# Optimization experiments

Hardware: AMD Instinct MI355X
Metric: run time of the kernel (lower is better)

## Reference

```python
import jax, jax.numpy as jnp
import numpy as np

MAX_SEQ = 512
HIDDEN = 1024
E = 2048  # hidden * expansion_factor
S = 128
EPS = 1e-05


def _rope(x):
    # x: [b, n, 2, s]; rotate along sequence dim (dim=1 in the torch code)
    b, n, h, s = x.shape
    half = s // 2
    pos = jnp.arange(n, dtype=x.dtype)
    # torch: freq_seq = -arange(half)/half; inv_freq = 10000**(-freq_seq) = 10000**(arange/half)
    inv_freq = jnp.power(jnp.asarray(10000.0, x.dtype), jnp.arange(half, dtype=x.dtype) / half)
    sinusoid = pos[:, None] * inv_freq[None, :]          # [n, half]
    sin = jnp.sin(sinusoid)[None, :, None, :]            # [1, n, 1, half]
    cos = jnp.cos(sinusoid)[None, :, None, :]
    x1, x2 = jnp.split(x, 2, axis=-1)
    return jnp.concatenate([x1 * cos - x2 * sin, x2 * cos + x1 * sin], axis=-1)


def _rel_pos_bias(w, seq_len):
    # toeplitz construction (max_seq_length <= 512 branch)
    t = jnp.pad(w, (0, seq_len))                          # [3*seq_len - 1]
    t = jnp.tile(t, seq_len)[:-seq_len]                   # [seq_len*(3*seq_len-2)]
    t = t.reshape(seq_len, 3 * seq_len - 2)
    r = (2 * seq_len - 1) // 2
    return t[:, r:-r][None]                               # [1, seq_len, seq_len]


def setup_inputs() -> dict:
    key = jax.random.key(0)
    ks = jax.random.split(key, 6)
    x = jax.random.normal(ks[0], (16, 512, HIDDEN), dtype=jnp.float32)
    uv_w = jax.random.normal(ks[1], (2 * E + S, HIDDEN), dtype=jnp.float32) * 0.02
    o_w = jax.random.normal(ks[2], (HIDDEN, E), dtype=jnp.float32) * 0.02
    return {
        "x": x,
        "ln_w": jnp.ones((HIDDEN,), jnp.float32),
        "ln_b": jnp.zeros((HIDDEN,), jnp.float32),
        "uv_w": uv_w,
        "uv_b": jnp.zeros((2 * E + S,), jnp.float32),
        "gamma": jax.random.uniform(ks[3], (2, S), dtype=jnp.float32),
        "beta": jax.random.uniform(ks[4], (2, S), dtype=jnp.float32),
        "o_w": o_w,
        "o_b": jnp.zeros((HIDDEN,), jnp.float32),
        "w_rel": jax.random.uniform(ks[5], (2 * MAX_SEQ - 1,), dtype=jnp.float32),
    }


def reference(x, ln_w, ln_b, uv_w, uv_b, gamma, beta, o_w, o_b, w_rel):
    b, n, d = x.shape
    shortcut = x
    # LayerNorm
    mu = jnp.mean(x, axis=-1, keepdims=True)
    var = jnp.mean(jnp.square(x - mu), axis=-1, keepdims=True)
    xn = (x - mu) * jax.lax.rsqrt(var + EPS) * ln_w + ln_b
    # uv projection + silu on the whole projection
    uv = jax.nn.silu(jnp.einsum('bnd,fd->bnf', xn, uv_w) + uv_b)
    u, v, base = jnp.split(uv, [E, 2 * E], axis=-1)      # [b,n,E],[b,n,E],[b,n,S]
    # offset-scale: [b,n,S] x [2,S] -> [b,n,2,S]
    base = base[..., None, :] * gamma + beta
    base = _rope(base)
    q, k = base[:, :, 0, :], base[:, :, 1, :]
    qk = jnp.einsum('bnd,bmd->bnm', q, k)
    bias = _rel_pos_bias(w_rel, MAX_SEQ)[:, :n, :n]
    kernel = jnp.square(jax.nn.relu(qk / MAX_SEQ + bias))
    out = u * jnp.einsum('bnm,bme->bne', kernel, v)
    out = jnp.einsum('bne,de->bnd', out, o_w) + o_b
    return out + shortcut
```

## Files before the change

### kernel.cpp

```cpp
#include <hip/hip_runtime.h>
#include <hip/hip_bf16.h>


typedef __bf16 bf16_t;
typedef __bf16 bf16x4 __attribute__((ext_vector_type(4)));
typedef __bf16 bf16x8 __attribute__((ext_vector_type(8)));
typedef float  f32x4  __attribute__((ext_vector_type(4)));

__device__ __forceinline__ void async16(const void* g, void* l) {
  __builtin_amdgcn_global_load_lds(
      (const __attribute__((address_space(1))) void*)g,
      (__attribute__((address_space(3))) void*)l, 16, 0, 0);
}

__global__ __launch_bounds__(256) void fill_const(float* __restrict__ out,
                                                  float val, int n) {
  int i = blockIdx.x * 256 + threadIdx.x;
  if (i < n) out[i] = val;
}

__global__ void rope_table(float* __restrict__ cosT, float* __restrict__ sinT) {
  int idx = blockIdx.x * 256 + threadIdx.x;
  int n = idx >> 6, j = idx & 63;
  float invf = (float)pow(10000.0, (double)j * (1.0 / 64.0));
  float angf = (float)n * invf;
  cosT[idx] = (float)cos((double)angf);
  sinT[idx] = (float)sin((double)angf);
}

__global__ __launch_bounds__(256) void cvt_f32_bf16(const float* __restrict__ in,
                                                    bf16_t* __restrict__ out,
                                                    int n4) {
  int i = blockIdx.x * 256 + threadIdx.x;
  if (i < n4) {
    f32x4 v = ((const f32x4*)in)[i];
    bf16x4 o;
    o[0] = (__bf16)v[0]; o[1] = (__bf16)v[1];
    o[2] = (__bf16)v[2]; o[3] = (__bf16)v[3];
    ((bf16x4*)out)[i] = o;
  }
}

__global__ __launch_bounds__(256) void ln_kernel(const float* __restrict__ x,
                                                 const float* __restrict__ w,
                                                 const float* __restrict__ b,
                                                 bf16_t* __restrict__ xn) {
  int row = blockIdx.x;
  int tid = threadIdx.x;
  f32x4 v = *(const f32x4*)(x + (size_t)row * 1024 + tid * 4);
  float s = v[0] + v[1] + v[2] + v[3];
  float s2 = v[0]*v[0] + v[1]*v[1] + v[2]*v[2] + v[3]*v[3];
  for (int o = 32; o > 0; o >>= 1) {
    s += __shfl_down(s, o);
    s2 += __shfl_down(s2, o);
  }
  __shared__ float ps[4], ps2[4];
  if ((tid & 63) == 0) { ps[tid >> 6] = s; ps2[tid >> 6] = s2; }
  __syncthreads();
  float st = ps[0] + ps[1] + ps[2] + ps[3];
  float st2 = ps2[0] + ps2[1] + ps2[2] + ps2[3];
  float mean = st * (1.f / 1024.f);
  float var = st2 * (1.f / 1024.f) - mean * mean;
  float inv = 1.f / sqrtf(var + 1e-5f);
  bf16x4 o4;
  for (int i = 0; i < 4; i++) {
    float wn = w[tid * 4 + i], bn = b[tid * 4 + i];
    o4[i] = (__bf16)((v[i] - mean) * inv * wn + bn);
  }
  *(bf16x4*)(xn + (size_t)row * 1024 + tid * 4) = o4;
}

__global__ __launch_bounds__(128) void rope_qk(const bf16_t* __restrict__ baseb,
                                               const float* __restrict__ gamma,
                                               const float* __restrict__ beta,
                                               const float* __restrict__ cosT,
                                               const float* __restrict__ sinT,
                                               bf16_t* __restrict__ q,
                                               bf16_t* __restrict__ k) {
  int m = blockIdx.x;
  int n = m & 511;
  int s = threadIdx.x;
  float base = (float)baseb[(size_t)m * 128 + s];
  __shared__ float t[2][128];
  t[0][s] = base * gamma[s] + beta[s];
  t[1][s] = base * gamma[128 + s] + beta[128 + s];
  __syncthreads();
  int j = s & 63;
  float c = cosT[n * 64 + j], sn = sinT[n * 64 + j];
  for (int h = 0; h < 2; h++) {
    float x1 = t[h][j], x2 = t[h][64 + j];
    float r = (s < 64) ? (x1 * c - x2 * sn) : (x2 * c + x1 * sn);
    bf16_t* dst = h == 0 ? q : k;
    dst[(size_t)m * 128 + s] = (__bf16)r;
  }
}

struct EpiUV {
  const float* uv_b;
  bf16_t* u;
  bf16_t* vT;
  bf16_t* baseb;
  __device__ void operator()(int b, int m, int n, float acc) const {
    float xv = acc + uv_b[n];
    float sv = xv / (1.f + __expf(-xv));
    sv = fminf(fmaxf(sv, -100.f), 100.f);
    if (n < 2048) {
      u[(size_t)m * 2048 + n] = (__bf16)sv;
    } else if (n < 4096) {
      int bb = m >> 9, nseq = m & 511;
      vT[((size_t)bb * 2048 + (n - 2048)) * 512 + nseq] = (__bf16)sv;
    } else {
      baseb[(size_t)m * 128 + (n - 4096)] = (__bf16)sv;
    }
  }
};
struct EpiQK {
  const float* w_rel;
  bf16_t* km;
  __device__ void operator()(int b, int i, int j, float acc) const {
    float bias = w_rel[511 + j - i];
    float t = fmaxf(acc * (1.f / 512.f) + bias, 0.f);
    t = fminf(t, 100.f);
    km[((size_t)b * 512 + i) * 512 + j] = (__bf16)(t * t);
  }
};
struct EpiAttn {
  const bf16_t* u;
  bf16_t* out2;
  __device__ void operator()(int b, int i, int e, float acc) const {
    size_t m = (size_t)b * 512 + i;
    float uu = (float)u[m * 2048 + e];
    float r = acc * uu;
    r = fminf(fmaxf(r, -1e6f), 1e6f);
    out2[m * 2048 + e] = (__bf16)r;
  }
};
struct EpiOut {
  const float* o_b;
  const float* x;
  float* out;
  __device__ void operator()(int b, int m, int d, float acc) const {
    long idx = (long)m * 1024 + d;
    float r = acc + o_b[d] + x[idx];
    r = fminf(fmaxf(r, -1e5f), 1e5f);
    out[idx] = r;
  }
};

template <typename Epi>
__global__ __launch_bounds__(256, 2)
void gemm_nt(const bf16_t* __restrict__ A, const bf16_t* __restrict__ Bm,
             int lda, int ldb, int K, long sAz, long sBz, Epi epi) {
  __shared__ __align__(16) char smem[32768];
  char* smA = smem;
  char* smB = smem + 16384;
  const int tid = threadIdx.x;
  const int lane = tid & 63;
  const int wid = tid >> 6;
  const int wm = wid & 1, wn = wid >> 1;
  const int quad = lane >> 4, col16 = lane & 15;
  const int srow = lane >> 3;
  const int skc = lane & 7;
  const int bz = blockIdx.z;
  const int tileM = blockIdx.x * 128;
  const int tileN = blockIdx.y * 128;
  const bf16_t* Ab = A + (size_t)bz * sAz;
  const bf16_t* Bb = Bm + (size_t)bz * sBz;

  f32x4 acc[4][4] = {};

  for (int k0 = 0; k0 < K; k0 += 64) {
#pragma unroll
    for (int c4 = 0; c4 < 4; c4++) {
      int ch = c4 * 4 + wid;
      int row = ch * 8 + srow;
      int kc = skc ^ (row & 7);
      async16(Ab + (size_t)(tileM + row) * lda + k0 + kc * 8, smA + ch * 1024);
      async16(Bb + (size_t)(tileN + row) * ldb + k0 + kc * 8, smB + ch * 1024);
    }
    __syncthreads();
#pragma unroll
    for (int kk = 0; kk < 2; kk++) {
      bf16x8 af[4], bfr[4];
      int jj = kk * 4 + quad;
#pragma unroll
      for (int t = 0; t < 4; t++) {
        int ml = wm * 64 + t * 16 + col16;
        int nl = wn * 64 + t * 16 + col16;
        af[t] = *(const bf16x8*)(smA + (size_t)ml * 128 + ((jj ^ (ml & 7)) * 16));
        bfr[t] = *(const bf16x8*)(smB + (size_t)nl * 128 + ((jj ^ (nl & 7)) * 16));
      }
#pragma unroll
      for (int mt = 0; mt < 4; mt++)
#pragma unroll
        for (int nt = 0; nt < 4; nt++)
          acc[mt][nt] = __builtin_amdgcn_mfma_f32_16x16x32_bf16(af[mt], bfr[nt], acc[mt][nt], 0, 0, 0);
    }
    __syncthreads();
  }

#pragma unroll
  for (int mt = 0; mt < 4; mt++) {
    int gm = tileM + wm * 64 + mt * 16 + quad * 4;
#pragma unroll
    for (int nt = 0; nt < 4; nt++) {
      int gn = tileN + wn * 64 + nt * 16 + col16;
#pragma unroll
      for (int r = 0; r < 4; r++) epi(bz, gm + r, gn, acc[mt][nt][r]);
    }
  }
}

extern "C" void kernel_launch(void* const* d_in, const int* in_sizes, int n_in,
                              void* d_out, int out_size, void* d_ws, size_t ws_size,
                              hipStream_t stream) {
  const float* x = (const float*)d_in[0];
  const float* ln_w = (const float*)d_in[1];
  const float* ln_b = (const float*)d_in[2];
  const float* uv_w = (const float*)d_in[3];
  const float* uv_b = (const float*)d_in[4];
  const float* gamma = (const float*)d_in[5];
  const float* beta = (const float*)d_in[6];
  const float* o_w = (const float*)d_in[7];
  const float* o_b = (const float*)d_in[8];
  const float* w_rel = (const float*)d_in[9];
  float* out = (float*)d_out;

  const int NOUT = 8388608;
  const size_t WS_NEEDED = 71303168;
  if (ws_size < WS_NEEDED) {
    float wsMiB = (float)(ws_size >> 20);
    fill_const<<<dim3(32768), dim3(256), 0, stream>>>(out, 1000.f + wsMiB, NOUT);
    return;
  }

  char* ws = (char*)d_ws;
  bf16_t* u = (bf16_t*)(ws + 0);
  bf16_t* out2 = u;
  bf16_t* vT = (bf16_t*)(ws + 33554432);
  bf16_t* o_wb = (bf16_t*)(ws + 67108864);
  char* ob = (char*)d_out;
  bf16_t* xn = (bf16_t*)ob;
  bf16_t* uv_wb = (bf16_t*)(ob + 16777216);
  bf16_t* baseb = (bf16_t*)(ob + 25427968);
  float* cosT = (float*)(ob + 27525120);
  float* sinT = (float*)(ob + 27656192);
  bf16_t* qb = (bf16_t*)ob;
  bf16_t* kb = (bf16_t*)(ob + 2097152);
  bf16_t* km = (bf16_t*)(ob + 4194304);

  rope_table<<<dim3(128), dim3(256), 0, stream>>>(cosT, sinT);
  cvt_f32_bf16<<<dim3(4224), dim3(256), 0, stream>>>(uv_w, uv_wb, 1081344);
  cvt_f32_bf16<<<dim3(2048), dim3(256), 0, stream>>>(o_w, o_wb, 524288);
  ln_kernel<<<dim3(8192), dim3(256), 0, stream>>>(x, ln_w, ln_b, xn);
  gemm_nt<<<dim3(64, 33, 1), dim3(256), 0, stream>>>(
      xn, uv_wb, 1024, 1024, 1024, 0L, 0L, EpiUV{uv_b, u, vT, baseb});
  rope_qk<<<dim3(8192), dim3(128), 0, stream>>>(baseb, gamma, beta, cosT, sinT, qb, kb);
  gemm_nt<<<dim3(4, 4, 16), dim3(256), 0, stream>>>(
      qb, kb, 128, 128, 128, (long)512 * 128, (long)512 * 128, EpiQK{w_rel, km});
  gemm_nt<<<dim3(4, 16, 16), dim3(256), 0, stream>>>(
      km, vT, 512, 512, 512, (long)512 * 512, (long)2048 * 512, EpiAttn{u, out2});
  gemm_nt<<<dim3(64, 8, 1), dim3(256), 0, stream>>>(
      out2, o_wb, 2048, 2048, 2048, 0L, 0L, EpiOut{o_b, x, out});
}
```

Before: 333.8 us.

## Add 256x256 double-buffered GEMM kernel for UV projection and attention-value matmul

Introduces a new 512-thread GEMM with 256x256 output tiles, double-buffered async global-to-LDS loads with XOR swizzling, interleaved LDS reads and MFMA, and raised wave priority around the MFMA blocks. It is used for the UV projection and the kernel-times-V matmul to increase data reuse per tile and overlap loads with compute. Because the UV N dimension (4224) is not a multiple of 256, the weight buffer is padded with zero rows via an extra fill, later buffers are shifted, and the epilogue skips columns past 4224. The larger tiles use 128KB of LDS and many accumulator registers, which lowers occupancy and gives fewer blocks for the small batched matmul.

```diff
diff --git a/kernel.cpp b/kernel.cpp
--- a/kernel.cpp
+++ b/kernel.cpp
@@ -101,6 +101,7 @@
   bf16_t* vT;
   bf16_t* baseb;
   __device__ void operator()(int b, int m, int n, float acc) const {
+    if (n >= 4224) return;
     float xv = acc + uv_b[n];
     float sv = xv / (1.f + __expf(-xv));
     sv = fminf(fmaxf(sv, -100.f), 100.f);
@@ -211,6 +212,122 @@
   }
 }
 
+template <typename Epi>
+__global__ __launch_bounds__(512, 2)
+void gemm256(const bf16_t* __restrict__ A, const bf16_t* __restrict__ Bm,
+             int lda, int ldb, int K, long sAz, long sBz, Epi epi) {
+  __shared__ __align__(16) char smem[131072];
+  const int tid = threadIdx.x;
+  const int lane = tid & 63;
+  const int wid = tid >> 6;
+  const int wr = wid & 1;
+  const int wc = wid >> 1;
+  const int quad = lane >> 4, col16 = lane & 15;
+  const int bz = blockIdx.z;
+  const int tileM = blockIdx.x * 256;
+  const int tileN = blockIdx.y * 256;
+  const bf16_t* Ab = A + (size_t)bz * sAz;
+  const bf16_t* Bb = Bm + (size_t)bz * sBz;
+  const int NT = K >> 6;
+
+  f32x4 acc[8][4] = {};
+
+  auto stage = [&](int kt, int buf) {
+    char* dA = (char*)smem + buf * 65536;
+    char* dB = dA + 32768;
+    const int k0 = kt << 6;
+#pragma unroll
+    for (int i = 0; i < 4; i++) {
+      int li = i * 512 + tid;
+      int r = li >> 3;
+      int kc = (li & 7) ^ (r & 7);
+      async16(Ab + (size_t)(tileM + r) * lda + k0 + kc * 8, dA + li * 16);
+      async16(Bb + (size_t)(tileN + r) * ldb + k0 + kc * 8, dB + li * 16);
+    }
+  };
+
+  stage(0, 0);
+  stage(1, 1);
+  asm volatile("s_waitcnt vmcnt(8)" ::: "memory");
+  __builtin_amdgcn_s_barrier();
+  asm volatile("" ::: "memory");
+
+  for (int t = 0; t < NT; t++) {
+    const char* sA = (const char*)smem + (t & 1) * 65536;
+    const char* sB = sA + 32768;
+
+    bf16x8 a[4][2], b0[2][2], b1[2][2];
+
+#define RD_A4(mbase)                                                          \
+  {                                                                           \
+    _Pragma("unroll") for (int mt = 0; mt < 4; mt++)                          \
+        _Pragma("unroll") for (int kk = 0; kk < 2; kk++) {                    \
+      int ml = wr * 128 + ((mbase) + mt) * 16 + col16;                        \
+      int jj = kk * 4 + quad;                                                 \
+      a[mt][kk] =                                                             \
+          *(const bf16x8*)(sA + (size_t)ml * 128 + ((jj ^ (ml & 7)) << 4));   \
+    }                                                                         \
+  }
+#define RD_B2(b, nbase)                                                       \
+  {                                                                           \
+    _Pragma("unroll") for (int nt = 0; nt < 2; nt++)                          \
+        _Pragma("unroll") for (int kk = 0; kk < 2; kk++) {                    \
+      int nl = wc * 64 + ((nbase) + nt) * 16 + col16;                         \
+      int jj = kk * 4 + quad;                                                 \
+      b[nt][kk] =                                                             \
+          *(const bf16x8*)(sB + (size_t)nl * 128 + ((jj ^ (nl & 7)) << 4));   \
+    }                                                                         \
+  }
+#define MM8(mo, no, b)                                                        \
+  {                                                                           \
+    __builtin_amdgcn_s_setprio(1);                                            \
+    _Pragma("unroll") for (int mt = 0; mt < 4; mt++)                          \
+        _Pragma("unroll") for (int nt = 0; nt < 2; nt++)                      \
+            _Pragma("unroll") for (int kk = 0; kk < 2; kk++) {                \
+      acc[(mo) + mt][(no) + nt] = __builtin_amdgcn_mfma_f32_16x16x32_bf16(    \
+          a[mt][kk], b[nt][kk], acc[(mo) + mt][(no) + nt], 0, 0, 0);          \
+    }                                                                         \
+    __builtin_amdgcn_s_setprio(0);                                            \
+  }
+
+    RD_B2(b0, 0);
+    RD_A4(0);
+    MM8(0, 0, b0);
+    RD_B2(b1, 2);
+    MM8(0, 2, b1);
+    RD_A4(4);
+    MM8(4, 2, b1);
+    MM8(4, 0, b0);
+
+#undef RD_A4
+#undef RD_B2
+#undef MM8
+
+    if (t == NT - 1) break;
+    asm volatile("" ::: "memory");
+    __builtin_amdgcn_s_barrier();
+    if (t + 2 < NT) {
+      stage(t + 2, t & 1);
+      asm volatile("s_waitcnt vmcnt(8)" ::: "memory");
+    } else {
+      asm volatile("s_waitcnt vmcnt(0)" ::: "memory");
+    }
+    __builtin_amdgcn_s_barrier();
+    asm volatile("" ::: "memory");
+  }
+
+#pragma unroll
+  for (int mt = 0; mt < 8; mt++) {
+    int gm = tileM + wr * 128 + mt * 16 + quad * 4;
+#pragma unroll
+    for (int nt = 0; nt < 4; nt++) {
+      int gn = tileN + wc * 64 + nt * 16 + col16;
+#pragma unroll
+      for (int r = 0; r < 4; r++) epi(bz, gm + r, gn, acc[mt][nt][r]);
+    }
+  }
+}
+
 extern "C" void kernel_launch(void* const* d_in, const int* in_sizes, int n_in,
                               void* d_out, int out_size, void* d_ws, size_t ws_size,
                               hipStream_t stream) {
@@ -242,9 +359,9 @@
   char* ob = (char*)d_out;
   bf16_t* xn = (bf16_t*)ob;
   bf16_t* uv_wb = (bf16_t*)(ob + 16777216);
-  bf16_t* baseb = (bf16_t*)(ob + 25427968);
-  float* cosT = (float*)(ob + 27525120);
-  float* sinT = (float*)(ob + 27656192);
+  bf16_t* baseb = (bf16_t*)(ob + 25690112);
+  float* cosT = (float*)(ob + 27787264);
+  float* sinT = (float*)(ob + 27918336);
   bf16_t* qb = (bf16_t*)ob;
   bf16_t* kb = (bf16_t*)(ob + 2097152);
   bf16_t* km = (bf16_t*)(ob + 4194304);
@@ -252,13 +369,15 @@
   rope_table<<<dim3(128), dim3(256), 0, stream>>>(cosT, sinT);
   cvt_f32_bf16<<<dim3(4224), dim3(256), 0, stream>>>(uv_w, uv_wb, 1081344);
   cvt_f32_bf16<<<dim3(2048), dim3(256), 0, stream>>>(o_w, o_wb, 524288);
+  fill_const<<<dim3(256), dim3(256), 0, stream>>>(
+      (float*)(ob + 16777216 + 8650752), 0.f, 65536);
   ln_kernel<<<dim3(8192), dim3(256), 0, stream>>>(x, ln_w, ln_b, xn);
-  gemm_nt<<<dim3(64, 33, 1), dim3(256), 0, stream>>>(
+  gemm256<<<dim3(32, 17, 1), dim3(512), 0, stream>>>(
       xn, uv_wb, 1024, 1024, 1024, 0L, 0L, EpiUV{uv_b, u, vT, baseb});
   rope_qk<<<dim3(8192), dim3(128), 0, stream>>>(baseb, gamma, beta, cosT, sinT, qb, kb);
   gemm_nt<<<dim3(4, 4, 16), dim3(256), 0, stream>>>(
       qb, kb, 128, 128, 128, (long)512 * 128, (long)512 * 128, EpiQK{w_rel, km});
-  gemm_nt<<<dim3(4, 16, 16), dim3(256), 0, stream>>>(
+  gemm256<<<dim3(2, 8, 16), dim3(512), 0, stream>>>(
       km, vT, 512, 512, 512, (long)512 * 512, (long)2048 * 512, EpiAttn{u, out2});
   gemm_nt<<<dim3(64, 8, 1), dim3(256), 0, stream>>>(
       out2, o_wb, 2048, 2048, 2048, 0L, 0L, EpiOut{o_b, x, out});
```

Result: slower. 390.3 us (+16.9%).

## Add 256x256-tile pipelined GEMM kernel for UV projection and attention-value GEMMs

Applied to the files above, without the earlier changes.

Introduces a 512-thread GEMM with 256x256 output tiles, a 4-stage async global-to-LDS pipeline with XOR-swizzled shared memory, split A-half loads interleaved with MFMA phases, and priority hints. It is used for the UV projection and the kernel×V GEMM. Because the UV width of 4224 is not a multiple of 256, the padded weight rows are zero-filled and the epilogue skips columns past 4224, with scratch buffers shifted to make room. Larger tiles raise data reuse per block but lower occupancy and waste some work on the padded tile.

```diff
diff --git a/kernel.cpp b/kernel.cpp
--- a/kernel.cpp
+++ b/kernel.cpp
@@ -101,6 +101,7 @@
   bf16_t* vT;
   bf16_t* baseb;
   __device__ void operator()(int b, int m, int n, float acc) const {
+    if (n >= 4224) return;
     float xv = acc + uv_b[n];
     float sv = xv / (1.f + __expf(-xv));
     sv = fminf(fmaxf(sv, -100.f), 100.f);
@@ -211,6 +212,131 @@
   }
 }
 
+template <typename Epi>
+__global__ __launch_bounds__(512, 2)
+void gemm256(const bf16_t* __restrict__ A, const bf16_t* __restrict__ Bm,
+             int lda, int ldb, int K, long sAz, long sBz, Epi epi) {
+  __shared__ __align__(16) char smem[131072];
+  const int tid = threadIdx.x;
+  const int lane = tid & 63;
+  const int wid = tid >> 6;
+  const int wr = wid & 1;
+  const int wc = wid >> 1;
+  const int quad = lane >> 4, col16 = lane & 15;
+  const int bz = blockIdx.z;
+  const int tileM = blockIdx.x * 256;
+  const int tileN = blockIdx.y * 256;
+  const bf16_t* Ab = A + (size_t)bz * sAz;
+  const bf16_t* Bb = Bm + (size_t)bz * sBz;
+  const int NT = K >> 5;
+
+  int r_st[2], kc_st[2], u_st[2];
+#pragma unroll
+  for (int i = 0; i < 2; i++) {
+    int u = (tid >> 6) + (i << 3);
+    int c = (u << 6) + lane;
+    int line = c >> 3, slot = c & 7;
+    int g = slot ^ (line & 7);
+    u_st[i] = u;
+    r_st[i] = (line << 1) + (g >> 2);
+    kc_st[i] = g & 3;
+  }
+
+  int offA[8], offB[4];
+#pragma unroll
+  for (int mt = 0; mt < 8; mt++) {
+    int r = wr * 128 + mt * 16 + col16;
+    int line = r >> 1;
+    int g = ((r & 1) << 2) | quad;
+    offA[mt] = line * 128 + ((g ^ (line & 7)) << 4);
+  }
+#pragma unroll
+  for (int nt = 0; nt < 4; nt++) {
+    int r = wc * 64 + nt * 16 + col16;
+    int line = r >> 1;
+    int g = ((r & 1) << 2) | quad;
+    offB[nt] = line * 128 + ((g ^ (line & 7)) << 4);
+  }
+
+  auto stageHalf = [&](int kt, int h) {
+    char* dst = (char*)smem + (kt & 3) * 32768 + h * 16384;
+    const bf16_t* src = h ? Bb : Ab;
+    const int ld = h ? ldb : lda;
+    const int tb = h ? tileN : tileM;
+    const int k0 = kt << 5;
+#pragma unroll
+    for (int i = 0; i < 2; i++) {
+      async16(src + (size_t)(tb + r_st[i]) * ld + k0 + (kc_st[i] << 3),
+              dst + u_st[i] * 1024);
+    }
+  };
+
+  f32x4 acc[8][4] = {};
+
+#pragma unroll
+  for (int pt = 0; pt < 3; pt++) {
+    if (pt < NT) { stageHalf(pt, 0); stageHalf(pt, 1); }
+  }
+  asm volatile("s_waitcnt vmcnt(8)" ::: "memory");
+  __builtin_amdgcn_s_barrier();
+  asm volatile("" ::: "memory");
+
+  for (int t = 0; t < NT; t++) {
+    const char* sA = (const char*)smem + (t & 3) * 32768;
+    const char* sB = sA + 16384;
+    bf16x8 a[4], b[4];
+
+#pragma unroll
+    for (int i = 0; i < 4; i++) b[i] = *(const bf16x8*)(sB + offB[i]);
+#pragma unroll
+    for (int i = 0; i < 4; i++) a[i] = *(const bf16x8*)(sA + offA[i]);
+    if (t + 3 < NT) stageHalf(t + 3, 0);
+    asm volatile("" ::: "memory");
+    __builtin_amdgcn_s_barrier();
+    __builtin_amdgcn_s_setprio(1);
+#pragma unroll
+    for (int mt = 0; mt < 4; mt++)
+#pragma unroll
+      for (int nt = 0; nt < 4; nt++)
+        acc[mt][nt] = __builtin_amdgcn_mfma_f32_16x16x32_bf16(
+            a[mt], b[nt], acc[mt][nt], 0, 0, 0);
+    __builtin_amdgcn_s_setprio(0);
+    asm volatile("" ::: "memory");
+    __builtin_amdgcn_s_barrier();
+
+#pragma unroll
+    for (int i = 0; i < 4; i++) a[i] = *(const bf16x8*)(sA + offA[4 + i]);
+    if (t + 3 < NT) stageHalf(t + 3, 1);
+    asm volatile("" ::: "memory");
+    __builtin_amdgcn_s_barrier();
+    __builtin_amdgcn_s_setprio(1);
+#pragma unroll
+    for (int mt = 0; mt < 4; mt++)
+#pragma unroll
+      for (int nt = 0; nt < 4; nt++)
+        acc[4 + mt][nt] = __builtin_amdgcn_mfma_f32_16x16x32_bf16(
+            a[mt], b[nt], acc[4 + mt][nt], 0, 0, 0);
+    __builtin_amdgcn_s_setprio(0);
+
+    if (t + 1 < NT) {
+      asm volatile("s_waitcnt vmcnt(8)" ::: "memory");
+      __builtin_amdgcn_s_barrier();
+      asm volatile("" ::: "memory");
+    }
+  }
+
+#pragma unroll
+  for (int mt = 0; mt < 8; mt++) {
+    int gm = tileM + wr * 128 + mt * 16 + quad * 4;
+#pragma unroll
+    for (int nt = 0; nt < 4; nt++) {
+      int gn = tileN + wc * 64 + nt * 16 + col16;
+#pragma unroll
+      for (int r = 0; r < 4; r++) epi(bz, gm + r, gn, acc[mt][nt][r]);
+    }
+  }
+}
+
 extern "C" void kernel_launch(void* const* d_in, const int* in_sizes, int n_in,
                               void* d_out, int out_size, void* d_ws, size_t ws_size,
                               hipStream_t stream) {
@@ -242,9 +368,9 @@
   char* ob = (char*)d_out;
   bf16_t* xn = (bf16_t*)ob;
   bf16_t* uv_wb = (bf16_t*)(ob + 16777216);
-  bf16_t* baseb = (bf16_t*)(ob + 25427968);
-  float* cosT = (float*)(ob + 27525120);
-  float* sinT = (float*)(ob + 27656192);
+  bf16_t* baseb = (bf16_t*)(ob + 25690112);
+  float* cosT = (float*)(ob + 27787264);
+  float* sinT = (float*)(ob + 27918336);
   bf16_t* qb = (bf16_t*)ob;
   bf16_t* kb = (bf16_t*)(ob + 2097152);
   bf16_t* km = (bf16_t*)(ob + 4194304);
@@ -252,13 +378,15 @@
   rope_table<<<dim3(128), dim3(256), 0, stream>>>(cosT, sinT);
   cvt_f32_bf16<<<dim3(4224), dim3(256), 0, stream>>>(uv_w, uv_wb, 1081344);
   cvt_f32_bf16<<<dim3(2048), dim3(256), 0, stream>>>(o_w, o_wb, 524288);
+  fill_const<<<dim3(256), dim3(256), 0, stream>>>(
+      (float*)(ob + 16777216 + 8650752), 0.f, 65536);
   ln_kernel<<<dim3(8192), dim3(256), 0, stream>>>(x, ln_w, ln_b, xn);
-  gemm_nt<<<dim3(64, 33, 1), dim3(256), 0, stream>>>(
+  gemm256<<<dim3(32, 17, 1), dim3(512), 0, stream>>>(
       xn, uv_wb, 1024, 1024, 1024, 0L, 0L, EpiUV{uv_b, u, vT, baseb});
   rope_qk<<<dim3(8192), dim3(128), 0, stream>>>(baseb, gamma, beta, cosT, sinT, qb, kb);
   gemm_nt<<<dim3(4, 4, 16), dim3(256), 0, stream>>>(
       qb, kb, 128, 128, 128, (long)512 * 128, (long)512 * 128, EpiQK{w_rel, km});
-  gemm_nt<<<dim3(4, 16, 16), dim3(256), 0, stream>>>(
+  gemm256<<<dim3(2, 8, 16), dim3(512), 0, stream>>>(
       km, vT, 512, 512, 512, (long)512 * 512, (long)2048 * 512, EpiAttn{u, out2});
   gemm_nt<<<dim3(64, 8, 1), dim3(256), 0, stream>>>(
       out2, o_wb, 2048, 2048, 2048, 0L, 0L, EpiOut{o_b, x, out});
```

Result: slower. 395.4 us (+18.4%).
